# Kernel optimization log

Hardware: AMD Instinct MI355X
Metric: run time of the kernel (lower is better)

Reference implementation:

```python
import jax, jax.numpy as jnp
import numpy as np

N_ENT = 50000
N_EDGE = 500000
D = 256          # ent_hidden_size
H1, C1 = 8, 64   # conv1: heads=8, out=64, concat -> 512
NEG_SLOPE = 0.2
LN_EPS = 1e-5


def setup_inputs() -> dict:
    key = jax.random.key(0)
    ks = jax.random.split(key, 12)
    s = 0.05  # small init scale for numerical sanity
    return {
        "edge_index": jax.random.randint(ks[0], (2, N_EDGE), 0, N_ENT),
        "x": jax.random.normal(ks[1], (N_ENT, D), dtype=jnp.float32),
        "ln_w": jnp.ones((D,), jnp.float32),
        "ln_b": jnp.zeros((D,), jnp.float32),
        "W1": jax.random.normal(ks[2], (D, H1 * C1), dtype=jnp.float32) * s,
        "att_src1": jax.random.normal(ks[3], (H1, C1), dtype=jnp.float32) * s,
        "att_dst1": jax.random.normal(ks[4], (H1, C1), dtype=jnp.float32) * s,
        "b1": jnp.zeros((H1 * C1,), jnp.float32),
        "W2": jax.random.normal(ks[5], (H1 * C1, D), dtype=jnp.float32) * s,
        "att_src2": jax.random.normal(ks[6], (1, D), dtype=jnp.float32) * s,
        "att_dst2": jax.random.normal(ks[7], (1, D), dtype=jnp.float32) * s,
        "b2": jnp.zeros((D,), jnp.float32),
    }


def _gat_conv(x, edge_index, W, att_src, att_dst, bias, heads, out_ch, concat):
    """PyG GATConv (shared src/dst lin, add_self_loops=True, eval-mode dropout)."""
    n = x.shape[0]
    loops = jnp.arange(n)
    src = jnp.concatenate([edge_index[0], loops])  # [E+N]
    dst = jnp.concatenate([edge_index[1], loops])

    h = (x @ W).reshape(n, heads, out_ch)                 # [N,H,C]
    a_src = jnp.sum(h * att_src[None], axis=-1)           # [N,H]
    a_dst = jnp.sum(h * att_dst[None], axis=-1)           # [N,H]

    e = jax.nn.leaky_relu(a_src[src] + a_dst[dst], NEG_SLOPE)  # [E+N,H]
    # per-destination segment softmax (every dst has a self-loop -> no empties)
    m = jax.lax.stop_gradient(jax.ops.segment_max(e, dst, num_segments=n))
    p = jnp.exp(e - m[dst])
    denom = jax.ops.segment_sum(p, dst, num_segments=n)
    alpha = p / denom[dst]                                # [E+N,H]

    out = jax.ops.segment_sum(h[src] * alpha[..., None], dst, num_segments=n)  # [N,H,C]
    out = out.reshape(n, heads * out_ch) if concat else out.mean(axis=1)
    return out + bias


def reference(edge_index, x, ln_w, ln_b, W1, att_src1, att_dst1, b1,
              W2, att_src2, att_dst2, b2):
    # LayerNorm(ent_hidden), eps=1e-5; dropouts are eval-mode no-ops
    mu = jnp.mean(x, axis=-1, keepdims=True)
    var = jnp.var(x, axis=-1, keepdims=True)
    h = (x - mu) / jnp.sqrt(var + LN_EPS) * ln_w + ln_b
    h = jax.nn.elu(_gat_conv(h, edge_index, W1, att_src1, att_dst1, b1, H1, C1, True))
    return _gat_conv(h, edge_index, W2, att_src2, att_dst2, b2, 1, D, False)
```

## Files before the change

kernel.cpp:

```cpp
#include <hip/hip_runtime.h>
#include <hip/hip_bf16.h>
#include <cstdint>

#define N_ENT  50000
#define N_EDGE 500000
#define D_IN   256
constexpr int ETOT = N_EDGE + N_ENT;

typedef __attribute__((ext_vector_type(8))) short bfrag;
typedef __attribute__((ext_vector_type(4))) float f4acc;
typedef __attribute__((ext_vector_type(4))) float f32x4;
typedef __attribute__((ext_vector_type(8))) short s16x8;

__device__ __forceinline__ float lrelu(float x) { return x > 0.f ? x : 0.2f * x; }
__device__ __forceinline__ float eluf(float x)  { return x > 0.f ? x : (expf(x) - 1.f); }
__device__ __forceinline__ short to_bf16(float f) {
    __hip_bfloat16 b = __float2bfloat16(f);
    return *(short*)&b;
}
__device__ __forceinline__ float2 bf2_to_f32(unsigned int u) {
    float2 r;
    r.x = __uint_as_float(u << 16);
    r.y = __uint_as_float(u & 0xffff0000u);
    return r;
}

__global__ __launch_bounds__(256) void prep_kernel(const float* __restrict__ x,
        const float* __restrict__ lnw, const float* __restrict__ lnb,
        short* __restrict__ y, const int* __restrict__ ei, int* __restrict__ cnt,
        const float* __restrict__ W1, short* __restrict__ W1T,
        const float* __restrict__ W2, short* __restrict__ W2T)
{
    int blk = blockIdx.x;
    if (blk < 12500) {
        int n = blk * 4 + (threadIdx.x >> 6);
        int lane = threadIdx.x & 63;
        const f32x4 v = __builtin_nontemporal_load((const f32x4*)(x + (size_t)n * D_IN + lane * 4));
        float s  = v.x + v.y + v.z + v.w;
        float sq = v.x*v.x + v.y*v.y + v.z*v.z + v.w*v.w;
        #pragma unroll
        for (int off = 1; off < 64; off <<= 1) {
            s  += __shfl_xor(s, off);
            sq += __shfl_xor(sq, off);
        }
        float mean = s * (1.f / 256.f);
        float var  = sq * (1.f / 256.f) - mean * mean;
        float rstd = rsqrtf(var + 1e-5f);
        float4 wv = *(const float4*)(lnw + lane * 4);
        float4 bv = *(const float4*)(lnb + lane * 4);
        short4 o;
        o.x = to_bf16((v.x - mean) * rstd * wv.x + bv.x);
        o.y = to_bf16((v.y - mean) * rstd * wv.y + bv.y);
        o.z = to_bf16((v.z - mean) * rstd * wv.z + bv.z);
        o.w = to_bf16((v.w - mean) * rstd * wv.w + bv.w);
        *(short4*)(y + (size_t)n * D_IN + lane * 4) = o;
    } else if (blk < 14454) {
        int e = (blk - 12500) * 256 + threadIdx.x;
        if (e < N_EDGE) atomicAdd(&cnt[ei[N_EDGE + e]], 1);
    } else if (blk < 14966) {
        int i = (blk - 14454) * 256 + threadIdx.x;
        int r = i >> 9, c = i & 511;
        W1T[c * 256 + r] = to_bf16(W1[i]);
    } else {
        int i = (blk - 14966) * 256 + threadIdx.x;
        int r = i >> 8, c = i & 255;
        W2T[c * 512 + r] = to_bf16(W2[i]);
    }
}

template<int NN, int KK, int CH, bool DO_FILL>
__global__ __launch_bounds__(256) void gemm_mfma(const short* __restrict__ A,
        const short* __restrict__ BT, short* __restrict__ C,
        const float* __restrict__ att_s, const float* __restrict__ att_d,
        float* __restrict__ a_s, float* __restrict__ a_d, int M, int nGemm,
        const int* __restrict__ ei, const int* __restrict__ row_start,
        int* __restrict__ cursor2, int* __restrict__ csr_src)
{
    constexpr int GX = NN / 128;
    __shared__ short As[128 * 32];
    __shared__ short Bs[128 * 32];

    if (DO_FILL && (int)blockIdx.x >= nGemm) {
        int e = ((int)blockIdx.x - nGemm) * 256 + threadIdx.x;
        if (e < N_EDGE) {
            int d = ei[N_EDGE + e];
            int pos = atomicAdd(&cursor2[d], 1);
            csr_src[row_start[d] + pos] = ei[e];
        }
        return;
    }

    const int tid  = threadIdx.x;
    const int w    = tid >> 6;
    const int l    = tid & 63;
    const int wm   = w >> 1, wn = w & 1;
    const int m0   = ((int)blockIdx.x / GX) * 128;
    const int n0   = ((int)blockIdx.x % GX) * 128;
    const int quad = l >> 4;
    const int ln16 = l & 15;
    const int rl   = l >> 2;
    const int cs   = l & 3;

    f4acc acc[4][4];
    #pragma unroll
    for (int i = 0; i < 4; ++i)
        #pragma unroll
        for (int j = 0; j < 4; ++j)
            acc[i][j] = (f4acc){0.f, 0.f, 0.f, 0.f};

    for (int k0 = 0; k0 < KK; k0 += 32) {
        __syncthreads();
        #pragma unroll
        for (int tt = 0; tt < 2; ++tt) {
            int t   = w * 2 + tt;
            int row = t * 16 + rl;
            int ca  = cs ^ ((row >> 1) & 3);
            const short* ga = A + (size_t)(m0 + row) * KK + k0 + ca * 8;
            __builtin_amdgcn_global_load_lds(
                (const __attribute__((address_space(1))) unsigned int*)ga,
                (__attribute__((address_space(3))) unsigned int*)&As[t * 512], 16, 0, 0);
            const short* gb = BT + (size_t)(n0 + row) * KK + k0 + ca * 8;
            __builtin_amdgcn_global_load_lds(
                (const __attribute__((address_space(1))) unsigned int*)gb,
                (__attribute__((address_space(3))) unsigned int*)&Bs[t * 512], 16, 0, 0);
        }
        __syncthreads();
        bfrag af[4], bf[4];
        #pragma unroll
        for (int i = 0; i < 4; ++i) {
            int r = wm * 64 + i * 16 + ln16;
            af[i] = *(const bfrag*)&As[r * 32 + (quad ^ ((r >> 1) & 3)) * 8];
            int rn = wn * 64 + i * 16 + ln16;
            bf[i] = *(const bfrag*)&Bs[rn * 32 + (quad ^ ((rn >> 1) & 3)) * 8];
        }
        #pragma unroll
        for (int i = 0; i < 4; ++i)
            #pragma unroll
            for (int j = 0; j < 4; ++j)
                acc[i][j] = __builtin_amdgcn_mfma_f32_16x16x32_bf16(af[i], bf[j], acc[i][j], 0, 0, 0);
    }

    float as_c[4], ad_c[4];
    if constexpr (CH > 0) {
        #pragma unroll
        for (int j = 0; j < 4; ++j) {
            int gc = n0 + wn * 64 + j * 16 + ln16;
            as_c[j] = att_s[gc];
            ad_c[j] = att_d[gc];
        }
    }
    const int hh = (n0 + wn * 64) >> 6;

    #pragma unroll
    for (int i = 0; i < 4; ++i) {
        #pragma unroll
        for (int p = 0; p < 4; ++p) {
            int gr = m0 + wm * 64 + i * 16 + quad * 4 + p;
            float ps = 0.f, pd = 0.f;
            if constexpr (CH > 0) {
                #pragma unroll
                for (int j = 0; j < 4; ++j) {
                    float c = acc[i][j][p];
                    ps = fmaf(c, as_c[j], ps);
                    pd = fmaf(c, ad_c[j], pd);
                }
                #pragma unroll
                for (int off = 1; off < 16; off <<= 1) {
                    ps += __shfl_xor(ps, off);
                    pd += __shfl_xor(pd, off);
                }
            }
            if (gr < M) {
                #pragma unroll
                for (int j = 0; j < 4; ++j) {
                    int gc = n0 + wn * 64 + j * 16 + ln16;
                    C[(size_t)gr * NN + gc] = to_bf16(acc[i][j][p]);
                }
                if constexpr (CH == 64) {
                    if (ln16 == 0) {
                        a_s[(size_t)gr * (NN / 64) + hh] = ps;
                        a_d[(size_t)gr * (NN / 64) + hh] = pd;
                    }
                } else if constexpr (CH == 256) {
                    if (ln16 == 0) {
                        unsafeAtomicAdd(&a_s[gr], ps);
                        unsafeAtomicAdd(&a_d[gr], pd);
                    }
                }
            }
        }
    }
}

__global__ __launch_bounds__(256) void alloc_kernel(const int* __restrict__ cnt,
        int* __restrict__ row_start, int* __restrict__ cursor)
{
    int d = blockIdx.x * 256 + threadIdx.x;
    int lane = threadIdx.x & 63;
    int c = (d < N_ENT) ? cnt[d] : 0;
    int inc = c;
    #pragma unroll
    for (int off = 1; off < 64; off <<= 1) {
        int nb = __shfl_up(inc, off);
        if (lane >= off) inc += nb;
    }
    int waveTotal = __shfl(inc, 63);
    int base = 0;
    if (lane == 63) base = atomicAdd(cursor, waveTotal);
    base = __shfl(base, 63);
    if (d < N_ENT) row_start[d] = base + inc - c;
}

__global__ __launch_bounds__(256) void aggr1_kernel(const int* __restrict__ csr_src,
        const int* __restrict__ row_start, const int* __restrict__ cnt,
        const short* __restrict__ feat, const float* __restrict__ a_s,
        const float* __restrict__ a_d, const float* __restrict__ bias,
        short* __restrict__ out)
{
    int d = blockIdx.x * 4 + (threadIdx.x >> 6);
    if (d >= N_ENT) return;
    int lane = threadIdx.x & 63;
    int f0 = lane * 8;
    int h = lane >> 3;
    int rs = row_start[d];
    int n = cnt[d];
    float adh = a_d[d * 8 + h];

    float den = 0.f;
    float acc[8] = {0.f, 0.f, 0.f, 0.f, 0.f, 0.f, 0.f, 0.f};
    {
        float p = __expf(lrelu(a_s[d * 8 + h] + adh));
        den += p;
        uint4 rv = *(const uint4*)(feat + (size_t)d * 512 + f0);
        float2 t0 = bf2_to_f32(rv.x), t1 = bf2_to_f32(rv.y);
        float2 t2 = bf2_to_f32(rv.z), t3 = bf2_to_f32(rv.w);
        acc[0] += p * t0.x; acc[1] += p * t0.y; acc[2] += p * t1.x; acc[3] += p * t1.y;
        acc[4] += p * t2.x; acc[5] += p * t2.y; acc[6] += p * t3.x; acc[7] += p * t3.y;
    }
    int i = 0;
    for (; i + 4 <= n; i += 4) {
        int   sv[4];
        float ev[4];
        uint4 rv[4];
        #pragma unroll
        for (int u = 0; u < 4; ++u) sv[u] = csr_src[rs + i + u];
        #pragma unroll
        for (int u = 0; u < 4; ++u) ev[u] = a_s[sv[u] * 8 + h];
        #pragma unroll
        for (int u = 0; u < 4; ++u) rv[u] = *(const uint4*)(feat + (size_t)sv[u] * 512 + f0);
        #pragma unroll
        for (int u = 0; u < 4; ++u) {
            float p = __expf(lrelu(ev[u] + adh));
            den += p;
            float2 t0 = bf2_to_f32(rv[u].x), t1 = bf2_to_f32(rv[u].y);
            float2 t2 = bf2_to_f32(rv[u].z), t3 = bf2_to_f32(rv[u].w);
            acc[0] += p * t0.x; acc[1] += p * t0.y; acc[2] += p * t1.x; acc[3] += p * t1.y;
            acc[4] += p * t2.x; acc[5] += p * t2.y; acc[6] += p * t3.x; acc[7] += p * t3.y;
        }
    }
    for (; i < n; ++i) {
        int s = csr_src[rs + i];
        float p = __expf(lrelu(a_s[s * 8 + h] + adh));
        den += p;
        uint4 rv = *(const uint4*)(feat + (size_t)s * 512 + f0);
        float2 t0 = bf2_to_f32(rv.x), t1 = bf2_to_f32(rv.y);
        float2 t2 = bf2_to_f32(rv.z), t3 = bf2_to_f32(rv.w);
        acc[0] += p * t0.x; acc[1] += p * t0.y; acc[2] += p * t1.x; acc[3] += p * t1.y;
        acc[4] += p * t2.x; acc[5] += p * t2.y; acc[6] += p * t3.x; acc[7] += p * t3.y;
    }
    float inv = 1.f / den;
    float4 b0 = *(const float4*)(bias + f0);
    float4 b1 = *(const float4*)(bias + f0 + 4);
    s16x8 o;
    o[0] = to_bf16(eluf(acc[0] * inv + b0.x)); o[1] = to_bf16(eluf(acc[1] * inv + b0.y));
    o[2] = to_bf16(eluf(acc[2] * inv + b0.z)); o[3] = to_bf16(eluf(acc[3] * inv + b0.w));
    o[4] = to_bf16(eluf(acc[4] * inv + b1.x)); o[5] = to_bf16(eluf(acc[5] * inv + b1.y));
    o[6] = to_bf16(eluf(acc[6] * inv + b1.z)); o[7] = to_bf16(eluf(acc[7] * inv + b1.w));
    __builtin_nontemporal_store(o, (s16x8*)(out + (size_t)d * 512 + f0));
}

__global__ __launch_bounds__(256) void aggr2_kernel(const int* __restrict__ csr_src,
        const int* __restrict__ row_start, const int* __restrict__ cnt,
        const short* __restrict__ feat, const float* __restrict__ a_s,
        const float* __restrict__ a_d, const float* __restrict__ bias,
        float* __restrict__ out)
{
    int d = blockIdx.x * 4 + (threadIdx.x >> 6);
    if (d >= N_ENT) return;
    int lane = threadIdx.x & 63;
    int half = lane >> 5;
    int li   = lane & 31;
    int f0   = li * 8;
    int rs = row_start[d];
    int n = cnt[d];
    float adh = a_d[d];

    float den = 0.f;
    float acc[8] = {0.f, 0.f, 0.f, 0.f, 0.f, 0.f, 0.f, 0.f};
    {
        float p = (half == 0) ? __expf(lrelu(a_s[d] + adh)) : 0.f;
        uint4 rv = *(const uint4*)(feat + (size_t)d * 256 + f0);
        den += p;
        float2 t0 = bf2_to_f32(rv.x), t1 = bf2_to_f32(rv.y);
        float2 t2 = bf2_to_f32(rv.z), t3 = bf2_to_f32(rv.w);
        acc[0] += p * t0.x; acc[1] += p * t0.y; acc[2] += p * t1.x; acc[3] += p * t1.y;
        acc[4] += p * t2.x; acc[5] += p * t2.y; acc[6] += p * t3.x; acc[7] += p * t3.y;
    }
    int i = 0;
    for (; i + 4 <= n; i += 4) {
        int e0 = i + half, e1 = i + 2 + half;
        int s0 = csr_src[rs + e0];
        int s1 = csr_src[rs + e1];
        float a0 = a_s[s0], a1 = a_s[s1];
        uint4 rv0 = *(const uint4*)(feat + (size_t)s0 * 256 + f0);
        uint4 rv1 = *(const uint4*)(feat + (size_t)s1 * 256 + f0);
        float p0 = __expf(lrelu(a0 + adh));
        float p1 = __expf(lrelu(a1 + adh));
        den += p0 + p1;
        float2 t0, t1, t2, t3;
        t0 = bf2_to_f32(rv0.x); t1 = bf2_to_f32(rv0.y); t2 = bf2_to_f32(rv0.z); t3 = bf2_to_f32(rv0.w);
        acc[0] += p0 * t0.x; acc[1] += p0 * t0.y; acc[2] += p0 * t1.x; acc[3] += p0 * t1.y;
        acc[4] += p0 * t2.x; acc[5] += p0 * t2.y; acc[6] += p0 * t3.x; acc[7] += p0 * t3.y;
        t0 = bf2_to_f32(rv1.x); t1 = bf2_to_f32(rv1.y); t2 = bf2_to_f32(rv1.z); t3 = bf2_to_f32(rv1.w);
        acc[0] += p1 * t0.x; acc[1] += p1 * t0.y; acc[2] += p1 * t1.x; acc[3] += p1 * t1.y;
        acc[4] += p1 * t2.x; acc[5] += p1 * t2.y; acc[6] += p1 * t3.x; acc[7] += p1 * t3.y;
    }
    for (; i < n; i += 2) {
        int e = i + half;
        bool valid = e < n;
        int s = valid ? csr_src[rs + e] : d;
        float av = a_s[s];
        uint4 rv = *(const uint4*)(feat + (size_t)s * 256 + f0);
        float p = valid ? __expf(lrelu(av + adh)) : 0.f;
        den += p;
        float2 t0 = bf2_to_f32(rv.x), t1 = bf2_to_f32(rv.y);
        float2 t2 = bf2_to_f32(rv.z), t3 = bf2_to_f32(rv.w);
        acc[0] += p * t0.x; acc[1] += p * t0.y; acc[2] += p * t1.x; acc[3] += p * t1.y;
        acc[4] += p * t2.x; acc[5] += p * t2.y; acc[6] += p * t3.x; acc[7] += p * t3.y;
    }
    den += __shfl_xor(den, 32);
    #pragma unroll
    for (int k = 0; k < 8; ++k) acc[k] += __shfl_xor(acc[k], 32);

    float inv = 1.f / den;
    if (half == 0) {
        float4 b0 = *(const float4*)(bias + f0);
        float4 b1 = *(const float4*)(bias + f0 + 4);
        f32x4 o0, o1;
        o0.x = acc[0] * inv + b0.x; o0.y = acc[1] * inv + b0.y;
        o0.z = acc[2] * inv + b0.z; o0.w = acc[3] * inv + b0.w;
        o1.x = acc[4] * inv + b1.x; o1.y = acc[5] * inv + b1.y;
        o1.z = acc[6] * inv + b1.z; o1.w = acc[7] * inv + b1.w;
        __builtin_nontemporal_store(o0, (f32x4*)(out + (size_t)d * 256 + f0));
        __builtin_nontemporal_store(o1, (f32x4*)(out + (size_t)d * 256 + f0 + 4));
    }
}

extern "C" void kernel_launch(void* const* d_in, const int* in_sizes, int n_in,
                              void* d_out, int out_size, void* d_ws, size_t ws_size,
                              hipStream_t stream)
{
    const int*   ei     = (const int*)  d_in[0];
    const float* x      = (const float*)d_in[1];
    const float* ln_w   = (const float*)d_in[2];
    const float* ln_b   = (const float*)d_in[3];
    const float* W1     = (const float*)d_in[4];
    const float* att_s1 = (const float*)d_in[5];
    const float* att_d1 = (const float*)d_in[6];
    const float* b1     = (const float*)d_in[7];
    const float* W2     = (const float*)d_in[8];
    const float* att_s2 = (const float*)d_in[9];
    const float* att_d2 = (const float*)d_in[10];
    const float* b2     = (const float*)d_in[11];
    float* out = (float*)d_out;

    short* h0b = (short*)d_ws;
    short* h1b = h0b + 12800000;
    short* h2b = h1b + 25600000;
    short* h3b = h2b + 25600000;
    short* W1T = h3b + 12800000;
    short* W2T = W1T + 131072;
    float* a_s1 = (float*)(W2T + 131072);
    float* a_d1 = a_s1 + 400000;
    float* a_s2 = a_d1 + 400000;
    float* a_d2 = a_s2 + 50000;
    int* cnt       = (int*)(a_d2 + 50000);
    int* cursor2   = cnt + 50000;
    int* cursor    = cursor2 + 50000;
    int* row_start = cursor + 1;
    int* csr_src   = row_start + 50000;

    hipMemsetAsync(a_s2, 0, 200001 * 4, stream);

    prep_kernel<<<15478, 256, 0, stream>>>(x, ln_w, ln_b, h0b, ei, cnt, W1, W1T, W2, W2T);
    alloc_kernel<<<196, 256, 0, stream>>>(cnt, row_start, cursor);

    constexpr int NG1 = 391 * 4;
    gemm_mfma<512, 256, 64, true><<<NG1 + 1954, 256, 0, stream>>>(
        h0b, W1T, h1b, att_s1, att_d1, a_s1, a_d1, N_ENT, NG1,
        ei, row_start, cursor2, csr_src);
    aggr1_kernel<<<12500, 256, 0, stream>>>(csr_src, row_start, cnt, h1b, a_s1, a_d1, b1, h2b);

    constexpr int NG2 = 391 * 2;
    gemm_mfma<256, 512, 256, false><<<NG2, 256, 0, stream>>>(
        h2b, W2T, h3b, att_s2, att_d2, a_s2, a_d2, N_ENT, NG2,
        nullptr, nullptr, nullptr, nullptr);
    aggr2_kernel<<<12500, 256, 0, stream>>>(csr_src, row_start, cnt, h3b, a_s2, a_d2, b2, out);
}
```

Before: 391.3 us.

## Precompute W·att vectors to compute attention logits outside GEMM epilogues

Folds the attention vectors into the weight matrices (W1·att1 and W2·att2), so the per-node attention logits become small dot products with the GEMM input rather than reductions over the GEMM output. Layer-1 logits are computed by extra tail blocks in the first GEMM launch, and layer-2 logits are computed in the aggr1 epilogue from fp32 ELU outputs. This removes the shuffle reductions and the layer-2 float atomics from the GEMM epilogues, and drops the memset of a_s2/a_d2. In exchange the logits now come from bf16 inputs with fp32 fused weights instead of the fp32 accumulators, which changes rounding slightly, and the first GEMM launch gains extra blocks.

```diff
diff --git a/kernel.cpp b/kernel.cpp
--- a/kernel.cpp
+++ b/kernel.cpp
@@ -5,7 +5,6 @@
 #define N_ENT  50000
 #define N_EDGE 500000
 #define D_IN   256
-constexpr int ETOT = N_EDGE + N_ENT;
 
 typedef __attribute__((ext_vector_type(8))) short bfrag;
 typedef __attribute__((ext_vector_type(4))) float f4acc;
@@ -29,7 +28,10 @@
         const float* __restrict__ lnw, const float* __restrict__ lnb,
         short* __restrict__ y, const int* __restrict__ ei, int* __restrict__ cnt,
         const float* __restrict__ W1, short* __restrict__ W1T,
-        const float* __restrict__ W2, short* __restrict__ W2T)
+        const float* __restrict__ W2, short* __restrict__ W2T,
+        const float* __restrict__ att_s1, const float* __restrict__ att_d1,
+        const float* __restrict__ att_s2, const float* __restrict__ att_d2,
+        float* __restrict__ wAtt, float* __restrict__ v2s, float* __restrict__ v2d)
 {
     int blk = blockIdx.x;
     if (blk < 12500) {
@@ -61,31 +63,97 @@
         int i = (blk - 14454) * 256 + threadIdx.x;
         int r = i >> 9, c = i & 511;
         W1T[c * 256 + r] = to_bf16(W1[i]);
-    } else {
+    } else if (blk < 15478) {
         int i = (blk - 14966) * 256 + threadIdx.x;
         int r = i >> 8, c = i & 255;
         W2T[c * 512 + r] = to_bf16(W2[i]);
-    }
-}
-
-template<int NN, int KK, int CH, bool DO_FILL>
+    } else if (blk == 15478) {
+        int k = threadIdx.x;
+        const float* wrow = W1 + (size_t)k * 512;
+        #pragma unroll
+        for (int h = 0; h < 8; ++h) {
+            float ws = 0.f, wd = 0.f;
+            #pragma unroll
+            for (int c4 = 0; c4 < 16; ++c4) {
+                float4 wv = *(const float4*)(wrow + h * 64 + c4 * 4);
+                float4 as = *(const float4*)(att_s1 + h * 64 + c4 * 4);
+                float4 ad = *(const float4*)(att_d1 + h * 64 + c4 * 4);
+                ws += wv.x*as.x + wv.y*as.y + wv.z*as.z + wv.w*as.w;
+                wd += wv.x*ad.x + wv.y*ad.y + wv.z*ad.z + wv.w*ad.w;
+            }
+            wAtt[k * 16 + h]     = ws;
+            wAtt[k * 16 + 8 + h] = wd;
+        }
+    } else {
+        int t = threadIdx.x;
+        #pragma unroll
+        for (int kk = 0; kk < 2; ++kk) {
+            int k = t + kk * 256;
+            const float* wrow = W2 + (size_t)k * 256;
+            float vs = 0.f, vd = 0.f;
+            for (int c4 = 0; c4 < 64; ++c4) {
+                float4 wv = *(const float4*)(wrow + c4 * 4);
+                float4 as = *(const float4*)(att_s2 + c4 * 4);
+                float4 ad = *(const float4*)(att_d2 + c4 * 4);
+                vs += wv.x*as.x + wv.y*as.y + wv.z*as.z + wv.w*as.w;
+                vd += wv.x*ad.x + wv.y*ad.y + wv.z*ad.z + wv.w*ad.w;
+            }
+            v2s[k] = vs;
+            v2d[k] = vd;
+        }
+    }
+}
+
+template<int NN, int KK, bool TAIL>
 __global__ __launch_bounds__(256) void gemm_mfma(const short* __restrict__ A,
-        const short* __restrict__ BT, short* __restrict__ C,
-        const float* __restrict__ att_s, const float* __restrict__ att_d,
-        float* __restrict__ a_s, float* __restrict__ a_d, int M, int nGemm,
+        const short* __restrict__ BT, short* __restrict__ C, int M, int nGemm, int nFill,
         const int* __restrict__ ei, const int* __restrict__ row_start,
-        int* __restrict__ cursor2, int* __restrict__ csr_src)
+        int* __restrict__ cursor2, int* __restrict__ csr_src,
+        const float* __restrict__ wAtt, float* __restrict__ a_s, float* __restrict__ a_d)
 {
     constexpr int GX = NN / 128;
-    __shared__ short As[128 * 32];
-    __shared__ short Bs[128 * 32];
-
-    if (DO_FILL && (int)blockIdx.x >= nGemm) {
-        int e = ((int)blockIdx.x - nGemm) * 256 + threadIdx.x;
-        if (e < N_EDGE) {
-            int d = ei[N_EDGE + e];
-            int pos = atomicAdd(&cursor2[d], 1);
-            csr_src[row_start[d] + pos] = ei[e];
+    __shared__ __align__(16) short As[128 * 32];
+    __shared__ __align__(16) short Bs[128 * 32];
+
+    if (TAIL && (int)blockIdx.x >= nGemm) {
+        int bb = (int)blockIdx.x - nGemm;
+        if (bb < nFill) {
+            int e = bb * 256 + threadIdx.x;
+            if (e < N_EDGE) {
+                int d = ei[N_EDGE + e];
+                int pos = atomicAdd(&cursor2[d], 1);
+                csr_src[row_start[d] + pos] = ei[e];
+            }
+        } else {
+            float* wlo = (float*)As;
+            float* whi = (float*)Bs;
+            for (int i = threadIdx.x; i < 4096; i += 256) {
+                int o = i & 15, k = i >> 4;
+                if (o < 8) wlo[o * 256 + k] = wAtt[i];
+                else       whi[(o - 8) * 256 + k] = wAtt[i];
+            }
+            __syncthreads();
+            int lane = threadIdx.x & 63, w = threadIdx.x >> 6;
+            int r0 = (bb - nFill) * 32 + w * 8;
+            for (int it = 0; it < 8; ++it) {
+                int r = r0 + it;
+                if (r >= N_ENT) break;
+                uint2 hv = *(const uint2*)(A + (size_t)r * 256 + lane * 4);
+                float2 a01 = bf2_to_f32(hv.x), a23 = bf2_to_f32(hv.y);
+                float p[16];
+                #pragma unroll
+                for (int o = 0; o < 16; ++o) {
+                    const float* wb = (o < 8) ? &wlo[o * 256] : &whi[(o - 8) * 256];
+                    f32x4 wv = *(const f32x4*)&wb[lane * 4];
+                    p[o] = a01.x * wv.x + a01.y * wv.y + a23.x * wv.z + a23.y * wv.w;
+                }
+                #pragma unroll
+                for (int off = 1; off < 64; off <<= 1)
+                    #pragma unroll
+                    for (int o = 0; o < 16; ++o) p[o] += __shfl_xor(p[o], off);
+                if (lane < 8)       a_s[(size_t)r * 8 + lane] = p[lane];
+                else if (lane < 16) a_d[(size_t)r * 8 + lane - 8] = p[lane];
+            }
         }
         return;
     }
@@ -140,52 +208,16 @@
                 acc[i][j] = __builtin_amdgcn_mfma_f32_16x16x32_bf16(af[i], bf[j], acc[i][j], 0, 0, 0);
     }
 
-    float as_c[4], ad_c[4];
-    if constexpr (CH > 0) {
-        #pragma unroll
-        for (int j = 0; j < 4; ++j) {
-            int gc = n0 + wn * 64 + j * 16 + ln16;
-            as_c[j] = att_s[gc];
-            ad_c[j] = att_d[gc];
-        }
-    }
-    const int hh = (n0 + wn * 64) >> 6;
-
     #pragma unroll
     for (int i = 0; i < 4; ++i) {
         #pragma unroll
         for (int p = 0; p < 4; ++p) {
             int gr = m0 + wm * 64 + i * 16 + quad * 4 + p;
-            float ps = 0.f, pd = 0.f;
-            if constexpr (CH > 0) {
-                #pragma unroll
-                for (int j = 0; j < 4; ++j) {
-                    float c = acc[i][j][p];
-                    ps = fmaf(c, as_c[j], ps);
-                    pd = fmaf(c, ad_c[j], pd);
-                }
-                #pragma unroll
-                for (int off = 1; off < 16; off <<= 1) {
-                    ps += __shfl_xor(ps, off);
-                    pd += __shfl_xor(pd, off);
-                }
-            }
             if (gr < M) {
                 #pragma unroll
                 for (int j = 0; j < 4; ++j) {
                     int gc = n0 + wn * 64 + j * 16 + ln16;
                     C[(size_t)gr * NN + gc] = to_bf16(acc[i][j][p]);
-                }
-                if constexpr (CH == 64) {
-                    if (ln16 == 0) {
-                        a_s[(size_t)gr * (NN / 64) + hh] = ps;
-                        a_d[(size_t)gr * (NN / 64) + hh] = pd;
-                    }
-                } else if constexpr (CH == 256) {
-                    if (ln16 == 0) {
-                        unsafeAtomicAdd(&a_s[gr], ps);
-                        unsafeAtomicAdd(&a_d[gr], pd);
-                    }
                 }
             }
         }
@@ -215,7 +247,9 @@
         const int* __restrict__ row_start, const int* __restrict__ cnt,
         const short* __restrict__ feat, const float* __restrict__ a_s,
         const float* __restrict__ a_d, const float* __restrict__ bias,
-        short* __restrict__ out)
+        short* __restrict__ out,
+        const float* __restrict__ v2s, const float* __restrict__ v2d,
+        float* __restrict__ a_s2, float* __restrict__ a_d2)
 {
     int d = blockIdx.x * 4 + (threadIdx.x >> 6);
     if (d >= N_ENT) return;
@@ -271,11 +305,30 @@
     float inv = 1.f / den;
     float4 b0 = *(const float4*)(bias + f0);
     float4 b1 = *(const float4*)(bias + f0 + 4);
+    float hv[8];
+    hv[0] = eluf(acc[0] * inv + b0.x); hv[1] = eluf(acc[1] * inv + b0.y);
+    hv[2] = eluf(acc[2] * inv + b0.z); hv[3] = eluf(acc[3] * inv + b0.w);
+    hv[4] = eluf(acc[4] * inv + b1.x); hv[5] = eluf(acc[5] * inv + b1.y);
+    hv[6] = eluf(acc[6] * inv + b1.z); hv[7] = eluf(acc[7] * inv + b1.w);
+
+    float4 s0 = *(const float4*)(v2s + f0), s1 = *(const float4*)(v2s + f0 + 4);
+    float4 d0 = *(const float4*)(v2d + f0), d1 = *(const float4*)(v2d + f0 + 4);
+    float ds = hv[0]*s0.x + hv[1]*s0.y + hv[2]*s0.z + hv[3]*s0.w
+             + hv[4]*s1.x + hv[5]*s1.y + hv[6]*s1.z + hv[7]*s1.w;
+    float dd = hv[0]*d0.x + hv[1]*d0.y + hv[2]*d0.z + hv[3]*d0.w
+             + hv[4]*d1.x + hv[5]*d1.y + hv[6]*d1.z + hv[7]*d1.w;
+    #pragma unroll
+    for (int off = 1; off < 64; off <<= 1) {
+        ds += __shfl_xor(ds, off);
+        dd += __shfl_xor(dd, off);
+    }
+    if (lane == 0) { a_s2[d] = ds; a_d2[d] = dd; }
+
     s16x8 o;
-    o[0] = to_bf16(eluf(acc[0] * inv + b0.x)); o[1] = to_bf16(eluf(acc[1] * inv + b0.y));
-    o[2] = to_bf16(eluf(acc[2] * inv + b0.z)); o[3] = to_bf16(eluf(acc[3] * inv + b0.w));
-    o[4] = to_bf16(eluf(acc[4] * inv + b1.x)); o[5] = to_bf16(eluf(acc[5] * inv + b1.y));
-    o[6] = to_bf16(eluf(acc[6] * inv + b1.z)); o[7] = to_bf16(eluf(acc[7] * inv + b1.w));
+    o[0] = to_bf16(hv[0]); o[1] = to_bf16(hv[1]);
+    o[2] = to_bf16(hv[2]); o[3] = to_bf16(hv[3]);
+    o[4] = to_bf16(hv[4]); o[5] = to_bf16(hv[5]);
+    o[6] = to_bf16(hv[6]); o[7] = to_bf16(hv[7]);
     __builtin_nontemporal_store(o, (s16x8*)(out + (size_t)d * 512 + f0));
 }
 
@@ -384,26 +437,33 @@
     float* a_d1 = a_s1 + 400000;
     float* a_s2 = a_d1 + 400000;
     float* a_d2 = a_s2 + 50000;
-    int* cnt       = (int*)(a_d2 + 50000);
+    float* wAtt = a_d2 + 50000;
+    float* v2s  = wAtt + 4096;
+    float* v2d  = v2s + 512;
+    int* cnt       = (int*)(v2d + 512);
     int* cursor2   = cnt + 50000;
     int* cursor    = cursor2 + 50000;
     int* row_start = cursor + 1;
     int* csr_src   = row_start + 50000;
 
-    hipMemsetAsync(a_s2, 0, 200001 * 4, stream);
-
-    prep_kernel<<<15478, 256, 0, stream>>>(x, ln_w, ln_b, h0b, ei, cnt, W1, W1T, W2, W2T);
+    hipMemsetAsync(cnt, 0, 100001 * 4, stream);
+
+    prep_kernel<<<15480, 256, 0, stream>>>(x, ln_w, ln_b, h0b, ei, cnt, W1, W1T, W2, W2T,
+                                           att_s1, att_d1, att_s2, att_d2, wAtt, v2s, v2d);
     alloc_kernel<<<196, 256, 0, stream>>>(cnt, row_start, cursor);
 
     constexpr int NG1 = 391 * 4;
-    gemm_mfma<512, 256, 64, true><<<NG1 + 1954, 256, 0, stream>>>(
-        h0b, W1T, h1b, att_s1, att_d1, a_s1, a_d1, N_ENT, NG1,
-        ei, row_start, cursor2, csr_src);
-    aggr1_kernel<<<12500, 256, 0, stream>>>(csr_src, row_start, cnt, h1b, a_s1, a_d1, b1, h2b);
+    constexpr int NF1 = 1954;
+    constexpr int ND1 = 1563;
+    gemm_mfma<512, 256, true><<<NG1 + NF1 + ND1, 256, 0, stream>>>(
+        h0b, W1T, h1b, N_ENT, NG1, NF1,
+        ei, row_start, cursor2, csr_src, wAtt, a_s1, a_d1);
+    aggr1_kernel<<<12500, 256, 0, stream>>>(csr_src, row_start, cnt, h1b, a_s1, a_d1, b1, h2b,
+                                            v2s, v2d, a_s2, a_d2);
 
     constexpr int NG2 = 391 * 2;
-    gemm_mfma<256, 512, 256, false><<<NG2, 256, 0, stream>>>(
-        h2b, W2T, h3b, att_s2, att_d2, a_s2, a_d2, N_ENT, NG2,
-        nullptr, nullptr, nullptr, nullptr);
+    gemm_mfma<256, 512, false><<<NG2, 256, 0, stream>>>(
+        h2b, W2T, h3b, N_ENT, NG2, 0,
+        nullptr, nullptr, nullptr, nullptr, nullptr, nullptr, nullptr);
     aggr2_kernel<<<12500, 256, 0, stream>>>(csr_src, row_start, cnt, h3b, a_s2, a_d2, b2, out);
 }
```

After: 464.2 us. +18.6%, slower.
